# Kernel tuning notes

Measured on AMD Instinct MI355X. Metric: run time of the kernel, lower is better.

## Reference

```python
import jax, jax.numpy as jnp
import numpy as np

E, H, VOCAB = 32, 128, 32000
B, T = 32, 128


def _linear_params(key, out_f, in_f):
    kw, kb = jax.random.split(key)
    bound = 1.0 / np.sqrt(in_f)
    W = jax.random.uniform(kw, (out_f, in_f), jnp.float32, -bound, bound)
    b = jax.random.uniform(kb, (out_f,), jnp.float32, -bound, bound)
    return W, b


def setup_inputs() -> dict:
    key = jax.random.key(0)
    ks = jax.random.split(key, 10)
    x = jax.random.normal(ks[0], (B, T, E), jnp.float32)
    Wf, bWf = _linear_params(ks[1], H, E)
    Uf, bUf = _linear_params(ks[2], H, H)
    Wi, bWi = _linear_params(ks[3], H, E)
    Ui, bUi = _linear_params(ks[4], H, H)
    Wc, bWc = _linear_params(ks[5], H, E)
    Uc, bUc = _linear_params(ks[6], H, H)
    Wo, bWo = _linear_params(ks[7], H, E)
    Uo, bUo = _linear_params(ks[8], H, H)
    Vw, Vb = _linear_params(ks[9], VOCAB, H)
    return dict(x=x, Wf=Wf, bWf=bWf, Uf=Uf, bUf=bUf, Wi=Wi, bWi=bWi,
                Ui=Ui, bUi=bUi, Wc=Wc, bWc=bWc, Uc=Uc, bUc=bUc,
                Wo=Wo, bWo=bWo, Uo=Uo, bUo=bUo, Vw=Vw, Vb=Vb)


def _lstm_forward(x, Wf, bWf, Uf, bUf, Wi, bWi, Ui, bUi, Wc, bWc, Uc, bUc,
                  Wo, bWo, Uo, bUo, Vw, Vb):
    b = x.shape[0]
    # Precompute input-to-gate projections for all timesteps: [T, B, H] (time-major)
    xf = (jnp.einsum('bte,he->bth', x, Wf) + bWf).transpose(1, 0, 2)
    xi = (jnp.einsum('bte,he->bth', x, Wi) + bWi).transpose(1, 0, 2)
    xc = (jnp.einsum('bte,he->bth', x, Wc) + bWc).transpose(1, 0, 2)
    xo = (jnp.einsum('bte,he->bth', x, Wo) + bWo).transpose(1, 0, 2)

    h0 = jnp.zeros((b, H), x.dtype)
    c0 = jnp.zeros((b, H), x.dtype)

    def step(carry, xs):
        h, c = carry
        xf_t, xi_t, xc_t, xo_t = xs
        f = jax.nn.sigmoid(xf_t + h @ Uf.T + bUf)
        i = jax.nn.sigmoid(xi_t + h @ Ui.T + bUi)
        c_til = jnp.tanh(xc_t + h @ Uc.T + bUc)
        # Original module detaches the cell state before using it (self.ct = ct.detach())
        c_new = jax.lax.stop_gradient(f * c + i * c_til)
        o = jax.nn.sigmoid(xo_t + h @ Uo.T + bUo)
        h_new = o * jnp.tanh(c_new)
        out = h_new @ Vw.T + Vb  # [B, VOCAB]
        return (h_new, c_new), out

    (h_last, _), outs = jax.lax.scan(step, (h0, c0), (xf, xi, xc, xo))
    out_seq = outs.transpose(1, 0, 2)  # [B, T, VOCAB]
    return out_seq, h_last


def reference(x, Wf, bWf, Uf, bUf, Wi, bWi, Ui, bUi, Wc, bWc, Uc, bUc,
              Wo, bWo, Uo, bUo, Vw, Vb):
    return _lstm_forward(x, Wf, bWf, Uf, bUf, Wi, bWi, Ui, bUi, Wc, bWc,
                         Uc, bUc, Wo, bWo, Uo, bUo, Vw, Vb)
```

## Files before the change

### kernel.cpp

```cpp
#include <hip/hip_runtime.h>
#include <stdint.h>
#include <stddef.h>
#include <math.h>

#define E_ 32
#define H_ 128
#define V_ 32000
#define NB 32
#define NT 128
#define NCONS 224
#define NCHUNK 250
#define NX (NCHUNK - NCONS)
#define WSTEPS 16
#define NWIN (NT / WSTEPS)

typedef float f32x4 __attribute__((ext_vector_type(4)));
typedef short s16x8 __attribute__((ext_vector_type(8)));

__device__ inline unsigned short f2bf(float f) {
  uint32_t u = __float_as_uint(f);
  return (unsigned short)((u + 0x7FFFu + ((u >> 16) & 1u)) >> 16);
}

__device__ inline float dpp_xor1(float v) {
  return __int_as_float(__builtin_amdgcn_update_dpp(
      0, __float_as_int(v), 0xB1, 0xF, 0xF, true));
}
__device__ inline float dpp_xor2(float v) {
  return __int_as_float(__builtin_amdgcn_update_dpp(
      0, __float_as_int(v), 0x4E, 0xF, 0xF, true));
}

__global__ void zero_cnt(int* cnt) {
  if (threadIdx.x < NWIN) cnt[threadIdx.x] = 0;
}

__global__ __launch_bounds__(512, 1)
void lstm_fused(const float* __restrict__ x,
                const float* __restrict__ Wf, const float* __restrict__ bWf,
                const float* __restrict__ Uf, const float* __restrict__ bUf,
                const float* __restrict__ Wi, const float* __restrict__ bWi,
                const float* __restrict__ Ui, const float* __restrict__ bUi,
                const float* __restrict__ Wc, const float* __restrict__ bWc,
                const float* __restrict__ Uc, const float* __restrict__ bUc,
                const float* __restrict__ Wo, const float* __restrict__ bWo,
                const float* __restrict__ Uo, const float* __restrict__ bUo,
                const float* __restrict__ Vw, const float* __restrict__ Vb,
                unsigned short* __restrict__ hbf,
                int* __restrict__ cnt,
                float* __restrict__ out,
                float* __restrict__ hlast)
{
  __shared__ __align__(16) unsigned char smem[81920];
  const int bid = blockIdx.x;
  const int tid = threadIdx.x;

  if (bid < NB) {
    float* xs = reinterpret_cast<float*>(smem);
    float* hd = reinterpret_cast<float*>(smem + 16384);

    const int q  = tid & 3;
    const int jj = tid >> 2;

    const float* WL[4]  = {Wf, Wi, Wc, Wo};
    const float* UL[4]  = {Uf, Ui, Uc, Uo};
    const float* bWL[4] = {bWf, bWi, bWc, bWo};
    const float* bUL[4] = {bUf, bUi, bUc, bUo};

    f32x4 wr_[4][2];
    f32x4 ur_[4][8];
    float bias_[4];
#pragma unroll
    for (int g = 0; g < 4; ++g) {
      const f32x4* Wp = reinterpret_cast<const f32x4*>(WL[g] + jj * E_ + q * 8);
      wr_[g][0] = Wp[0]; wr_[g][1] = Wp[1];
      const f32x4* Up = reinterpret_cast<const f32x4*>(UL[g] + jj * H_ + q * 32);
#pragma unroll
      for (int r = 0; r < 8; ++r) ur_[g][r] = Up[r];
      bias_[g] = bWL[g][jj] + bUL[g][jj];
    }

    for (int i = tid; i < NT * E_; i += 512) xs[i] = x[bid * (NT * E_) + i];
    if (tid < 144) hd[tid] = 0.f;
    float creg = 0.f;
    __syncthreads();

    for (int t = 0; t < NT; ++t) {
      const int cur = t & 1, nxt = cur ^ 1;
      const f32x4* hq = reinterpret_cast<const f32x4*>(hd + cur * 144 + q * 36);
      const f32x4* xq = reinterpret_cast<const f32x4*>(xs + t * E_ + q * 8);

      f32x4 p0 = {0.f,0.f,0.f,0.f}, p1 = p0, p2 = p0, p3 = p0;
#pragma unroll
      for (int r = 0; r < 2; ++r) {
        f32x4 xv = xq[r];
        p0 += wr_[0][r] * xv; p1 += wr_[1][r] * xv;
        p2 += wr_[2][r] * xv; p3 += wr_[3][r] * xv;
      }
#pragma unroll
      for (int r = 0; r < 8; ++r) {
        f32x4 hv = hq[r];
        p0 += ur_[0][r] * hv; p1 += ur_[1][r] * hv;
        p2 += ur_[2][r] * hv; p3 += ur_[3][r] * hv;
      }
      float s0 = (p0.x + p0.y) + (p0.z + p0.w);
      float s1 = (p1.x + p1.y) + (p1.z + p1.w);
      float s2 = (p2.x + p2.y) + (p2.z + p2.w);
      float s3 = (p3.x + p3.y) + (p3.z + p3.w);
      s0 += dpp_xor1(s0); s0 += dpp_xor2(s0);
      s1 += dpp_xor1(s1); s1 += dpp_xor2(s1);
      s2 += dpp_xor1(s2); s2 += dpp_xor2(s2);
      s3 += dpp_xor1(s3); s3 += dpp_xor2(s3);
      s0 += bias_[0]; s1 += bias_[1]; s2 += bias_[2]; s3 += bias_[3];

      float own = (q == 0) ? s0 : (q == 1) ? s1 : (q == 2) ? s2 : s3;
      float xin = (q == 2) ? own + own : own;
      float val = __builtin_amdgcn_rcpf(1.f + __expf(-xin));
      if (q == 2) val = 2.f * val - 1.f;
      float v1 = dpp_xor1(val);
      float v2 = dpp_xor2(val);
      float v3 = dpp_xor2(v1);
      float f_ = (q == 0) ? val : (q == 1) ? v1 : (q == 2) ? v2 : v3;
      float i_ = (q == 0) ? v1 : (q == 1) ? val : (q == 2) ? v3 : v2;
      float c_ = (q == 0) ? v2 : (q == 1) ? v3 : (q == 2) ? val : v1;
      float o_ = (q == 0) ? v3 : (q == 1) ? v2 : (q == 2) ? v1 : val;

      float cn = f_ * creg + i_ * c_;
      creg = cn;
      float hn = o_ * (2.f * __builtin_amdgcn_rcpf(1.f + __expf(-2.f * cn)) - 1.f);

      if (q == 0) {
        hd[nxt * 144 + jj + ((jj >> 5) << 2)] = hn;
        hbf[((size_t)t * NB + bid) * H_ + jj] = f2bf(hn);
        if (t == NT - 1) hlast[bid * H_ + jj] = hn;
      }
      __syncthreads();
      if ((t & (WSTEPS - 1)) == (WSTEPS - 1) && tid == 0)
        __hip_atomic_fetch_add(&cnt[t / WSTEPS], 1, __ATOMIC_RELEASE,
                               __HIP_MEMORY_SCOPE_AGENT);
    }
    return;
  }

  const int cid = bid - NB;
  unsigned char* vwo = smem;
  unsigned char* vwx = smem + 32768;
  unsigned char* hlb = smem + 65536;

  const int w = tid >> 6, lane = tid & 63;
  const int wr = w & 1, wc = w >> 1;
  const int l15 = lane & 15, lh = lane >> 4;

  for (int u = tid; u < 2048; u += 512) {
    int n = u >> 4, kc = u & 15;
    const f32x4* src = reinterpret_cast<const f32x4*>(
        Vw + ((size_t)(cid * 128 + n)) * H_ + kc * 8);
    f32x4 a = src[0], b = src[1];
    s16x8 o;
    o[0] = (short)f2bf(a.x); o[1] = (short)f2bf(a.y);
    o[2] = (short)f2bf(a.z); o[3] = (short)f2bf(a.w);
    o[4] = (short)f2bf(b.x); o[5] = (short)f2bf(b.y);
    o[6] = (short)f2bf(b.z); o[7] = (short)f2bf(b.w);
    *reinterpret_cast<s16x8*>(vwo + n * 256 + ((kc * 16) ^ ((n & 7) << 4))) = o;
  }
  float vbo0 = Vb[cid * 128 + wc * 32 + l15];
  float vbo1 = Vb[cid * 128 + wc * 32 + 16 + l15];
  const int hb_ = tid >> 4, hkc_ = tid & 15;
  const int hswz = hb_ * 256 + ((hkc_ * 16) ^ ((hb_ & 7) << 4));
  __syncthreads();

  const int rb = wc * 32 + l15;
  s16x8 bO0[4], bO1[4];
#pragma unroll
  for (int kt = 0; kt < 4; ++kt) {
    bO0[kt] = *reinterpret_cast<const s16x8*>(
        vwo + rb * 256 + ((kt * 64 + lh * 16) ^ ((rb & 7) << 4)));
    bO1[kt] = *reinterpret_cast<const s16x8*>(
        vwo + (rb + 16) * 256 + ((kt * 64 + lh * 16) ^ (((rb + 16) & 7) << 4)));
  }

  s16x8 bX0[4], bX1[4];
  float vbx0 = 0.f, vbx1 = 0.f;

  for (int win = 0; win < NWIN; ++win) {
    if (tid == 0) {
      while (__hip_atomic_load(&cnt[win], __ATOMIC_RELAXED,
                               __HIP_MEMORY_SCOPE_AGENT) < NB)
        __builtin_amdgcn_s_sleep(8);
      (void)__hip_atomic_load(&cnt[win], __ATOMIC_ACQUIRE,
                              __HIP_MEMORY_SCOPE_AGENT);
    }
    __syncthreads();

    s16x8 hv = *reinterpret_cast<const s16x8*>(
        hbf + (size_t)(win * WSTEPS) * (NB * H_) + tid * 8);

    const int k = cid - NX * win;
    const bool duty = (k >= 0) && (k < NX);
    int chunk_x = NCONS + k;
    if (duty) {
      for (int u = tid; u < 2048; u += 512) {
        int n = u >> 4, kc = u & 15;
        const f32x4* src = reinterpret_cast<const f32x4*>(
            Vw + ((size_t)(chunk_x * 128 + n)) * H_ + kc * 8);
        f32x4 a = src[0], b = src[1];
        s16x8 o;
        o[0] = (short)f2bf(a.x); o[1] = (short)f2bf(a.y);
        o[2] = (short)f2bf(a.z); o[3] = (short)f2bf(a.w);
        o[4] = (short)f2bf(b.x); o[5] = (short)f2bf(b.y);
        o[6] = (short)f2bf(b.z); o[7] = (short)f2bf(b.w);
        *reinterpret_cast<s16x8*>(vwx + n * 256 + ((kc * 16) ^ ((n & 7) << 4))) = o;
      }
      vbx0 = Vb[chunk_x * 128 + wc * 32 + l15];
      vbx1 = Vb[chunk_x * 128 + wc * 32 + 16 + l15];
    }

    for (int tt = 0; tt < WSTEPS; ++tt) {
      const int t = win * WSTEPS + tt;
      unsigned char* hcur = hlb + (tt & 1) * 8192;
      *reinterpret_cast<s16x8*>(hcur + hswz) = hv;
      if (tt < WSTEPS - 1)
        hv = *reinterpret_cast<const s16x8*>(
            hbf + (size_t)(t + 1) * (NB * H_) + tid * 8);
      __syncthreads();

      if (tt == 0 && duty) {
#pragma unroll
        for (int kt = 0; kt < 4; ++kt) {
          bX0[kt] = *reinterpret_cast<const s16x8*>(
              vwx + rb * 256 + ((kt * 64 + lh * 16) ^ ((rb & 7) << 4)));
          bX1[kt] = *reinterpret_cast<const s16x8*>(
              vwx + (rb + 16) * 256 + ((kt * 64 + lh * 16) ^ (((rb + 16) & 7) << 4)));
        }
      }

      s16x8 af[4];
      const int ra = wr * 16 + l15;
#pragma unroll
      for (int kt = 0; kt < 4; ++kt)
        af[kt] = *reinterpret_cast<const s16x8*>(
            hcur + ra * 256 + ((kt * 64 + lh * 16) ^ ((ra & 7) << 4)));

      {
        f32x4 acc0 = {0.f,0.f,0.f,0.f}, acc1 = acc0;
#pragma unroll
        for (int kt = 0; kt < 4; ++kt) {
          acc0 = __builtin_amdgcn_mfma_f32_16x16x32_bf16(af[kt], bO0[kt], acc0, 0, 0, 0);
          acc1 = __builtin_amdgcn_mfma_f32_16x16x32_bf16(af[kt], bO1[kt], acc1, 0, 0, 0);
        }
        const int colbase = cid * 128 + wc * 32;
#pragma unroll
        for (int i = 0; i < 4; ++i) {
          int b = wr * 16 + lh * 4 + i;
          float* orow = out + ((size_t)b * NT + t) * V_ + colbase;
          orow[l15]      = acc0[i] + vbo0;
          orow[16 + l15] = acc1[i] + vbo1;
        }
      }
      if (duty) {
        f32x4 acc0 = {0.f,0.f,0.f,0.f}, acc1 = acc0;
#pragma unroll
        for (int kt = 0; kt < 4; ++kt) {
          acc0 = __builtin_amdgcn_mfma_f32_16x16x32_bf16(af[kt], bX0[kt], acc0, 0, 0, 0);
          acc1 = __builtin_amdgcn_mfma_f32_16x16x32_bf16(af[kt], bX1[kt], acc1, 0, 0, 0);
        }
        const int colbase = chunk_x * 128 + wc * 32;
#pragma unroll
        for (int i = 0; i < 4; ++i) {
          int b = wr * 16 + lh * 4 + i;
          float* orow = out + ((size_t)b * NT + t) * V_ + colbase;
          orow[l15]      = acc0[i] + vbx0;
          orow[16 + l15] = acc1[i] + vbx1;
        }
      }
    }
  }
}

extern "C" void kernel_launch(void* const* d_in, const int* in_sizes, int n_in,
                              void* d_out, int out_size, void* d_ws, size_t ws_size,
                              hipStream_t stream) {
  const float* x   = (const float*)d_in[0];
  const float* Wf  = (const float*)d_in[1];
  const float* bWf = (const float*)d_in[2];
  const float* Uf  = (const float*)d_in[3];
  const float* bUf = (const float*)d_in[4];
  const float* Wi  = (const float*)d_in[5];
  const float* bWi = (const float*)d_in[6];
  const float* Ui  = (const float*)d_in[7];
  const float* bUi = (const float*)d_in[8];
  const float* Wc  = (const float*)d_in[9];
  const float* bWc = (const float*)d_in[10];
  const float* Uc  = (const float*)d_in[11];
  const float* bUc = (const float*)d_in[12];
  const float* Wo  = (const float*)d_in[13];
  const float* bWo = (const float*)d_in[14];
  const float* Uo  = (const float*)d_in[15];
  const float* bUo = (const float*)d_in[16];
  const float* Vw  = (const float*)d_in[17];
  const float* Vb  = (const float*)d_in[18];
  float* out = (float*)d_out;

  unsigned short* hbf = (unsigned short*)d_ws;
  int* cnt = (int*)((char*)d_ws + (1u << 20));
  float* hlast = out + (size_t)NB * NT * V_;

  hipLaunchKernelGGL(zero_cnt, dim3(1), dim3(64), 0, stream, cnt);
  hipLaunchKernelGGL(lstm_fused, dim3(256), dim3(512), 0, stream,
                     x, Wf, bWf, Uf, bUf, Wi, bWi, Ui, bUi, Wc, bWc, Uc, bUc,
                     Wo, bWo, Uo, bUo, Vw, Vb, hbf, cnt, out, hlast);
}
```

Baseline: 157.7 us.

## Use per-wave private LDS h tiles to drop per-step block barrier

Consumer blocks now stage each wave's 16 rows of bf16 hidden state into a wave-private LDS region instead of a shared double buffer. This removes the block-wide __syncthreads between the h store and the MFMA A-fragment load at every timestep. The duty-chunk B-fragment loads move to window start behind one barrier. The cost is more LDS (96 KB), and each wave loads four times as much h from global memory, redundantly with the other waves that share its rows.

```diff
diff --git a/kernel.cpp b/kernel.cpp
--- a/kernel.cpp
+++ b/kernel.cpp
@@ -51,7 +51,7 @@
                 float* __restrict__ out,
                 float* __restrict__ hlast)
 {
-  __shared__ __align__(16) unsigned char smem[81920];
+  __shared__ __align__(16) unsigned char smem[98304];
   const int bid = blockIdx.x;
   const int tid = threadIdx.x;
 
@@ -145,11 +145,11 @@
   const int cid = bid - NB;
   unsigned char* vwo = smem;
   unsigned char* vwx = smem + 32768;
-  unsigned char* hlb = smem + 65536;
 
   const int w = tid >> 6, lane = tid & 63;
   const int wr = w & 1, wc = w >> 1;
   const int l15 = lane & 15, lh = lane >> 4;
+  unsigned char* hpw = smem + 65536 + w * 4096;
 
   for (int u = tid; u < 2048; u += 512) {
     int n = u >> 4, kc = u & 15;
@@ -165,8 +165,13 @@
   }
   float vbo0 = Vb[cid * 128 + wc * 32 + l15];
   float vbo1 = Vb[cid * 128 + wc * 32 + 16 + l15];
-  const int hb_ = tid >> 4, hkc_ = tid & 15;
-  const int hswz = hb_ * 256 + ((hkc_ * 16) ^ ((hb_ & 7) << 4));
+
+  const int prow = lane >> 2, pcb = (lane & 3) * 64;
+  const int psw = (prow & 7) << 4;
+  const int hoff0 = prow * 256 + ((pcb +  0) ^ psw);
+  const int hoff1 = prow * 256 + ((pcb + 16) ^ psw);
+  const int hoff2 = prow * 256 + ((pcb + 32) ^ psw);
+  const int hoff3 = prow * 256 + ((pcb + 48) ^ psw);
   __syncthreads();
 
   const int rb = wc * 32 + l15;
@@ -192,8 +197,12 @@
     }
     __syncthreads();
 
-    s16x8 hv = *reinterpret_cast<const s16x8*>(
-        hbf + (size_t)(win * WSTEPS) * (NB * H_) + tid * 8);
+    const unsigned short* hsl = hbf + (size_t)(win * WSTEPS) * (NB * H_)
+                                    + wr * 16 * H_ + lane * 32;
+    s16x8 hvA = *reinterpret_cast<const s16x8*>(hsl);
+    s16x8 hvB = *reinterpret_cast<const s16x8*>(hsl + 8);
+    s16x8 hvC = *reinterpret_cast<const s16x8*>(hsl + 16);
+    s16x8 hvD = *reinterpret_cast<const s16x8*>(hsl + 24);
 
     const int k = cid - NX * win;
     const bool duty = (k >= 0) && (k < NX);
@@ -213,33 +222,36 @@
       }
       vbx0 = Vb[chunk_x * 128 + wc * 32 + l15];
       vbx1 = Vb[chunk_x * 128 + wc * 32 + 16 + l15];
+      __syncthreads();
+#pragma unroll
+      for (int kt = 0; kt < 4; ++kt) {
+        bX0[kt] = *reinterpret_cast<const s16x8*>(
+            vwx + rb * 256 + ((kt * 64 + lh * 16) ^ ((rb & 7) << 4)));
+        bX1[kt] = *reinterpret_cast<const s16x8*>(
+            vwx + (rb + 16) * 256 + ((kt * 64 + lh * 16) ^ (((rb + 16) & 7) << 4)));
+      }
     }
 
     for (int tt = 0; tt < WSTEPS; ++tt) {
       const int t = win * WSTEPS + tt;
-      unsigned char* hcur = hlb + (tt & 1) * 8192;
-      *reinterpret_cast<s16x8*>(hcur + hswz) = hv;
-      if (tt < WSTEPS - 1)
-        hv = *reinterpret_cast<const s16x8*>(
-            hbf + (size_t)(t + 1) * (NB * H_) + tid * 8);
-      __syncthreads();
-
-      if (tt == 0 && duty) {
-#pragma unroll
-        for (int kt = 0; kt < 4; ++kt) {
-          bX0[kt] = *reinterpret_cast<const s16x8*>(
-              vwx + rb * 256 + ((kt * 64 + lh * 16) ^ ((rb & 7) << 4)));
-          bX1[kt] = *reinterpret_cast<const s16x8*>(
-              vwx + (rb + 16) * 256 + ((kt * 64 + lh * 16) ^ (((rb + 16) & 7) << 4)));
-        }
+      *reinterpret_cast<s16x8*>(hpw + hoff0) = hvA;
+      *reinterpret_cast<s16x8*>(hpw + hoff1) = hvB;
+      *reinterpret_cast<s16x8*>(hpw + hoff2) = hvC;
+      *reinterpret_cast<s16x8*>(hpw + hoff3) = hvD;
+      if (tt < WSTEPS - 1) {
+        const unsigned short* nsl = hbf + (size_t)(t + 1) * (NB * H_)
+                                        + wr * 16 * H_ + lane * 32;
+        hvA = *reinterpret_cast<const s16x8*>(nsl);
+        hvB = *reinterpret_cast<const s16x8*>(nsl + 8);
+        hvC = *reinterpret_cast<const s16x8*>(nsl + 16);
+        hvD = *reinterpret_cast<const s16x8*>(nsl + 24);
       }
 
       s16x8 af[4];
-      const int ra = wr * 16 + l15;
 #pragma unroll
       for (int kt = 0; kt < 4; ++kt)
         af[kt] = *reinterpret_cast<const s16x8*>(
-            hcur + ra * 256 + ((kt * 64 + lh * 16) ^ ((ra & 7) << 4)));
+            hpw + l15 * 256 + ((kt * 64 + lh * 16) ^ ((l15 & 7) << 4)));
 
       {
         f32x4 acc0 = {0.f,0.f,0.f,0.f}, acc1 = acc0;
```

Measured after the change: 165.1 us. 4.7% more time.
